# Kernel tuning notes

Hardware: AMD Instinct MI355X
Metric: run time of the kernel (lower is better)

Reference implementation:

```python
import jax, jax.numpy as jnp
import numpy as np

N = 20000      # nodes
E = 640000     # edges (avg degree 32)
H = 128        # hidden_channels
L = 12         # num_layers
DIN = 3        # node feature dim
DE = 4         # edge feature dim
DOUT = 16      # output dim (y_s size)
EPS = 1e-7     # GENConv message eps
LN_EPS = 1e-5


def setup_inputs() -> dict:
    key = jax.random.key(0)
    ks = jax.random.split(key, 12)

    def w(k, shape, fan_in):
        return (jax.random.normal(k, shape, dtype=jnp.float32) / np.float32(np.sqrt(fan_in)))

    return {
        "x": jax.random.normal(ks[0], (N, DIN), dtype=jnp.float32),
        "edge_index": jax.random.randint(ks[1], (2, E), 0, N, dtype=jnp.int32),
        "edge_attr": jax.random.uniform(ks[2], (E, DE), dtype=jnp.float32),
        "enc_node_w": w(ks[3], (DIN, H), DIN),
        "enc_node_b": jnp.zeros((H,), jnp.float32),
        "enc_edge_w": w(ks[4], (DE, H), DE),
        "enc_edge_b": jnp.zeros((H,), jnp.float32),
        "t": jnp.ones((L,), jnp.float32),                 # learnable softmax temperature per layer
        "mlp1_w": w(ks[5], (L, H, 2 * H), H),
        "mlp1_b": jnp.zeros((L, 2 * H), jnp.float32),
        "mlp_ln_g": jnp.ones((L, 2 * H), jnp.float32),
        "mlp_ln_b": jnp.zeros((L, 2 * H), jnp.float32),
        "mlp2_w": w(ks[6], (L, 2 * H, H), 2 * H),
        "mlp2_b": jnp.zeros((L, H), jnp.float32),
        "ln_g": jnp.ones((L, H), jnp.float32),            # DeepGCNLayer pre-norm params
        "ln_b": jnp.zeros((L, H), jnp.float32),
        "lin_w": w(ks[7], (H, DOUT), H),
        "lin_b": jnp.zeros((DOUT,), jnp.float32),
    }


def _layer_norm(x, g, b):
    mu = jnp.mean(x, axis=-1, keepdims=True)
    var = jnp.mean(jnp.square(x - mu), axis=-1, keepdims=True)
    return (x - mu) * jax.lax.rsqrt(var + LN_EPS) * g + b


def _genconv(h, src, dst, ea, ti, w1, b1, g1, bb1, w2, b2):
    # message: relu(x_j + edge_attr) + eps  -> [E, H]
    m = jax.nn.relu(h[src] + ea) + EPS
    # learnable-temperature softmax over edges grouped by destination node
    logits = m * ti
    mx = jax.ops.segment_max(logits, dst, num_segments=N)
    mx = jnp.where(jnp.isfinite(mx), mx, 0.0)  # guard empty segments
    ex = jnp.exp(logits - mx[dst])
    den = jax.ops.segment_sum(ex, dst, num_segments=N) + 1e-16
    agg = jax.ops.segment_sum(m * (ex / den[dst]), dst, num_segments=N)
    # GENConv update: out = MLP(agg + x) with MLP = Lin(H,2H)->LN->ReLU->Lin(2H,H)
    out = agg + h
    u = jax.nn.relu(_layer_norm(out @ w1 + b1, g1, bb1))
    return u @ w2 + b2


def reference(x, edge_index, edge_attr, enc_node_w, enc_node_b, enc_edge_w,
              enc_edge_b, t, mlp1_w, mlp1_b, mlp_ln_g, mlp_ln_b, mlp2_w,
              mlp2_b, ln_g, ln_b, lin_w, lin_b):
    src, dst = edge_index[0], edge_index[1]
    h = x @ enc_node_w + enc_node_b            # node encoder
    ea = edge_attr @ enc_edge_w + enc_edge_b   # edge encoder

    # first layer: conv only (no norm/act, no residual)
    h = _genconv(h, src, dst, ea, t[0], mlp1_w[0], mlp1_b[0], mlp_ln_g[0],
                 mlp_ln_b[0], mlp2_w[0], mlp2_b[0])

    # remaining layers: res+ block  x = x + conv(relu(norm(x)))
    for i in range(1, L):
        hn = jax.nn.relu(_layer_norm(h, ln_g[i], ln_b[i]))
        h = h + _genconv(hn, src, dst, ea, t[i], mlp1_w[i], mlp1_b[i],
                         mlp_ln_g[i], mlp_ln_b[i], mlp2_w[i], mlp2_b[i])

    # final: layers[0].act(layers[0].norm(x)) then output linear
    h = jax.nn.relu(_layer_norm(h, ln_g[0], ln_b[0]))
    return h @ lin_w + lin_b
```

## Files before the change

### kernel.cpp

```cpp
#include <hip/hip_runtime.h>
#include <hip/hip_bf16.h>
#include <math.h>

#define NN 20000
#define EE 640000
#define HH 128
#define LL 12
#define DOUT_ 16
#define EPS_ 1e-7f
#define LN_EPS_ 1e-5f

typedef unsigned short u16;
typedef unsigned int u32;
typedef __attribute__((ext_vector_type(8))) short bf16x8;
typedef __attribute__((ext_vector_type(4))) float f32x4;

__device__ inline u16 bf16_rne(float v) {
  u32 u = __float_as_uint(v);
  return (u16)((u + 0x7FFFu + ((u >> 16) & 1u)) >> 16);
}
__device__ inline float bf16_tof(u16 h) { return __uint_as_float(((u32)h) << 16); }

__global__ __launch_bounds__(256) void hist_kernel(const int* __restrict__ dst, int* __restrict__ deg) {
  int e = blockIdx.x * 256 + threadIdx.x;
  if (e < EE) atomicAdd(&deg[dst[e]], 1);
}

__global__ __launch_bounds__(1024) void scan_kernel(const int* __restrict__ deg, int* __restrict__ off,
                                                    int* __restrict__ cur) {
  __shared__ int part[1024];
  int tid = threadIdx.x;
  const int CH = (NN + 1023) >> 10;
  int base = tid * CH;
  int s = 0;
  for (int j = 0; j < CH; ++j) { int i = base + j; if (i < NN) s += deg[i]; }
  part[tid] = s;
  __syncthreads();
  for (int d = 1; d < 1024; d <<= 1) {
    int v = (tid >= d) ? part[tid - d] : 0;
    __syncthreads();
    part[tid] += v;
    __syncthreads();
  }
  int run = part[tid] - s;
  for (int j = 0; j < CH; ++j) {
    int i = base + j;
    if (i < NN) { off[i] = run; cur[i] = run; run += deg[i]; }
  }
  if (tid == 1023) off[NN] = part[1023];
}

__global__ __launch_bounds__(256) void scatter_kernel(const int* __restrict__ src, const int* __restrict__ dst,
                                                      const float4* __restrict__ ea, int* __restrict__ cur,
                                                      int* __restrict__ srcs, float4* __restrict__ ea4) {
  int e = blockIdx.x * 256 + threadIdx.x;
  if (e >= EE) return;
  int d = dst[e];
  int p = atomicAdd(&cur[d], 1);
  srcs[p] = src[e];
  ea4[p] = ea[e];
}

__global__ __launch_bounds__(256) void wpack_kernel(const float* __restrict__ w, u16* __restrict__ dh,
                                                    u16* __restrict__ dl, int K, int N, int KSC) {
  int fid = blockIdx.x * 256 + threadIdx.x;
  int perL = (K * N) >> 3;
  if (fid >= LL * perL) return;
  int l = fid / perL, r = fid % perL;
  int lane = r & 63;
  int r2 = r >> 6;
  int ks2 = r2 % KSC; r2 /= KSC;
  int NT = N >> 4;
  int tI = r2 % NT;
  int chunk = r2 / NT;
  int c16 = lane & 15, kg = lane >> 4;
  int n = tI * 16 + c16;
  int k0 = (chunk * KSC + ks2) * 32 + kg * 8;
  const float* ws = w + (size_t)l * K * N;
  u16* oh = dh + (size_t)fid * 8;
  u16* ol = dl + (size_t)fid * 8;
  #pragma unroll
  for (int j = 0; j < 8; ++j) {
    float v = ws[(size_t)(k0 + j) * N + n];
    u16 hi = bf16_rne(v);
    oh[j] = hi;
    ol[j] = bf16_rne(v - bf16_tof(hi));
  }
}

__global__ __launch_bounds__(256) void encoder_kernel(const float* __restrict__ x, const float* __restrict__ w,
                                                      const float* __restrict__ b, float* __restrict__ h,
                                                      u16* __restrict__ hb) {
  int id = blockIdx.x * 256 + threadIdx.x;
  if (id >= NN * 64) return;
  int n = id >> 6, cp = id & 63;
  int c0 = cp * 2;
  float x0 = x[n*3+0], x1 = x[n*3+1], x2 = x[n*3+2];
  float vx = b[c0]   + x0*w[c0]   + x1*w[HH+c0]   + x2*w[2*HH+c0];
  float vy = b[c0+1] + x0*w[c0+1] + x1*w[HH+c0+1] + x2*w[2*HH+c0+1];
  *(float2*)&h[(size_t)n*HH + c0] = make_float2(vx, vy);
  *(u32*)&hb[(size_t)n*HH + c0] = (u32)bf16_rne(vx) | ((u32)bf16_rne(vy) << 16);
}

__global__ __launch_bounds__(256) void conv_kernel(const float* __restrict__ hn,
                                                   const u16* __restrict__ hb,
                                                   const int* __restrict__ off,
                                                   const int* __restrict__ srcs, const float4* __restrict__ ea4,
                                                   const float* __restrict__ eew, const float* __restrict__ eeb,
                                                   const float* __restrict__ t, int layer,
                                                   u16* __restrict__ tmpH, u16* __restrict__ tmpL) {
  int wid = blockIdx.x * 4 + (threadIdx.x >> 6);
  int lane = threadIdx.x & 63;
  if (wid >= NN) return;
  int c0 = lane * 2;
  float ti = t[layer];
  float w0x = eew[c0],      w0y = eew[c0+1];
  float w1x = eew[HH+c0],   w1y = eew[HH+c0+1];
  float w2x = eew[2*HH+c0], w2y = eew[2*HH+c0+1];
  float w3x = eew[3*HH+c0], w3y = eew[3*HH+c0+1];
  float bx = eeb[c0], by = eeb[c0+1];
  int e0 = off[wid], e1 = off[wid+1];
  float2 hd = *(const float2*)&hn[(size_t)wid*HH + c0];
  float den0 = 0.f, den1 = 0.f, num0 = 0.f, num1 = 0.f;

  int e = e0;
  const int UF = 8;
  for (; e + UF <= e1; e += UF) {
    int si[UF]; float4 av[UF];
    #pragma unroll
    for (int u = 0; u < UF; ++u) { si[u] = srcs[e + u]; av[u] = ea4[e + u]; }
    u32 hv[UF];
    #pragma unroll
    for (int u = 0; u < UF; ++u) hv[u] = *(const u32*)&hb[((u32)si[u] << 7) + c0];
    #pragma unroll
    for (int u = 0; u < UF; ++u) {
      float hx = bf16_tof((u16)(hv[u] & 0xffffu));
      float hy = bf16_tof((u16)(hv[u] >> 16));
      float eax = fmaf(av[u].w, w3x, fmaf(av[u].z, w2x, fmaf(av[u].y, w1x, fmaf(av[u].x, w0x, bx))));
      float eay = fmaf(av[u].w, w3y, fmaf(av[u].z, w2y, fmaf(av[u].y, w1y, fmaf(av[u].x, w0y, by))));
      float m0 = fmaxf(hx + eax, 0.f) + EPS_;
      float m1 = fmaxf(hy + eay, 0.f) + EPS_;
      float p0 = __expf(m0 * ti);
      float p1 = __expf(m1 * ti);
      den0 += p0; den1 += p1;
      num0 = fmaf(m0, p0, num0);
      num1 = fmaf(m1, p1, num1);
    }
  }
  for (; e < e1; ++e) {
    int sidx = srcs[e];
    float4 a = ea4[e];
    u32 hv = *(const u32*)&hb[((u32)sidx << 7) + c0];
    float hx = bf16_tof((u16)(hv & 0xffffu));
    float hy = bf16_tof((u16)(hv >> 16));
    float eax = fmaf(a.w, w3x, fmaf(a.z, w2x, fmaf(a.y, w1x, fmaf(a.x, w0x, bx))));
    float eay = fmaf(a.w, w3y, fmaf(a.z, w2y, fmaf(a.y, w1y, fmaf(a.x, w0y, by))));
    float m0 = fmaxf(hx + eax, 0.f) + EPS_;
    float m1 = fmaxf(hy + eay, 0.f) + EPS_;
    float p0 = __expf(m0 * ti);
    float p1 = __expf(m1 * ti);
    den0 += p0; den1 += p1;
    num0 = fmaf(m0, p0, num0);
    num1 = fmaf(m1, p1, num1);
  }
  float v0 = num0 / (den0 + 1e-16f) + hd.x;
  float v1 = num1 / (den1 + 1e-16f) + hd.y;
  u16 h0 = bf16_rne(v0), h1 = bf16_rne(v1);
  u16 l0 = bf16_rne(v0 - bf16_tof(h0)), l1 = bf16_rne(v1 - bf16_tof(h1));
  *(u32*)&tmpH[(size_t)wid*HH + c0] = (u32)h0 | ((u32)h1 << 16);
  *(u32*)&tmpL[(size_t)wid*HH + c0] = (u32)l0 | ((u32)l1 << 16);
}

__global__ __launch_bounds__(256) void gemm1_mfma(const u16* __restrict__ Ah, const u16* __restrict__ Al,
                                                  const u16* __restrict__ Bh, const u16* __restrict__ Bl,
                                                  const float* __restrict__ bias,
                                                  const float* __restrict__ g, const float* __restrict__ bb,
                                                  u16* __restrict__ Uh) {
  __shared__ u16 Bs[2][16384];
  int tid = threadIdx.x;
  int wv = tid >> 6, lane = tid & 63;
  int c16 = lane & 15, kg = lane >> 4;
  int row0 = blockIdx.x * 64 + wv * 16;
  int arow = row0 + c16; if (arow > NN - 1) arow = NN - 1;
  const u16* pAh = Ah + (size_t)arow * HH + kg * 8;
  const u16* pAl = Al + (size_t)arow * HH + kg * 8;
  f32x4 acc[16];
  #pragma unroll
  for (int tI = 0; tI < 16; ++tI) acc[tI] = (f32x4){0.f, 0.f, 0.f, 0.f};

  #pragma unroll
  for (int chunk = 0; chunk < 2; ++chunk) {
    const u16* sh = Bh + chunk * 16384;
    const u16* sl = Bl + chunk * 16384;
    #pragma unroll
    for (int it = 0; it < 8; ++it) {
      int idx = (it * 256 + tid) * 8;
      *(f32x4*)&Bs[0][idx] = *(const f32x4*)&sh[idx];
      *(f32x4*)&Bs[1][idx] = *(const f32x4*)&sl[idx];
    }
    __syncthreads();
    #pragma unroll
    for (int ks2 = 0; ks2 < 2; ++ks2) {
      int ks = chunk * 2 + ks2;
      bf16x8 ah = *(const bf16x8*)(pAh + ks * 32);
      bf16x8 al = *(const bf16x8*)(pAl + ks * 32);
      #pragma unroll
      for (int tI = 0; tI < 16; ++tI) {
        int boff = ((tI * 2 + ks2) * 64 + lane) * 8;
        bf16x8 bh = *(const bf16x8*)&Bs[0][boff];
        bf16x8 bl = *(const bf16x8*)&Bs[1][boff];
        acc[tI] = __builtin_amdgcn_mfma_f32_16x16x32_bf16(ah, bh, acc[tI], 0, 0, 0);
        acc[tI] = __builtin_amdgcn_mfma_f32_16x16x32_bf16(al, bh, acc[tI], 0, 0, 0);
        acc[tI] = __builtin_amdgcn_mfma_f32_16x16x32_bf16(ah, bl, acc[tI], 0, 0, 0);
      }
    }
    __syncthreads();
  }

  float bv[16], gv[16], bbv[16];
  #pragma unroll
  for (int tI = 0; tI < 16; ++tI) {
    int c = tI * 16 + c16;
    bv[tI] = bias[c]; gv[tI] = g[c]; bbv[tI] = bb[c];
  }
  #pragma unroll
  for (int j = 0; j < 4; ++j) {
    int row = row0 + kg * 4 + j;
    float xv[16], s = 0.f;
    #pragma unroll
    for (int tI = 0; tI < 16; ++tI) { xv[tI] = acc[tI][j] + bv[tI]; s += xv[tI]; }
    for (int m = 1; m <= 8; m <<= 1) s += __shfl_xor(s, m);
    float mu = s * (1.f / 256.f);
    float q = 0.f;
    #pragma unroll
    for (int tI = 0; tI < 16; ++tI) { xv[tI] -= mu; q += xv[tI] * xv[tI]; }
    for (int m = 1; m <= 8; m <<= 1) q += __shfl_xor(q, m);
    float rs = rsqrtf(q * (1.f / 256.f) + LN_EPS_);
    if (row < NN) {
      #pragma unroll
      for (int tI = 0; tI < 16; ++tI) {
        float o = fmaxf(xv[tI] * rs * gv[tI] + bbv[tI], 0.f);
        Uh[(size_t)row * 256 + tI * 16 + c16] = bf16_rne(o);
      }
    }
  }
}

__global__ __launch_bounds__(256) void gemm2_mfma(const u16* __restrict__ Ah,
                                                  const u16* __restrict__ Bh, const u16* __restrict__ Bl,
                                                  const float* __restrict__ bias,
                                                  const float* __restrict__ gn, const float* __restrict__ bn,
                                                  float* __restrict__ h, float* __restrict__ hnb,
                                                  u16* __restrict__ hb, int first) {
  __shared__ u16 Bs[2][16384];
  int tid = threadIdx.x;
  int wv = tid >> 6, lane = tid & 63;
  int c16 = lane & 15, kg = lane >> 4;
  int row0 = blockIdx.x * 64 + wv * 16;
  int arow = row0 + c16; if (arow > NN - 1) arow = NN - 1;
  const u16* pAh = Ah + (size_t)arow * 256 + kg * 8;
  f32x4 acc[8];
  #pragma unroll
  for (int tI = 0; tI < 8; ++tI) acc[tI] = (f32x4){0.f, 0.f, 0.f, 0.f};

  #pragma unroll
  for (int chunk = 0; chunk < 2; ++chunk) {
    const u16* sh = Bh + chunk * 16384;
    const u16* sl = Bl + chunk * 16384;
    #pragma unroll
    for (int it = 0; it < 8; ++it) {
      int idx = (it * 256 + tid) * 8;
      *(f32x4*)&Bs[0][idx] = *(const f32x4*)&sh[idx];
      *(f32x4*)&Bs[1][idx] = *(const f32x4*)&sl[idx];
    }
    __syncthreads();
    #pragma unroll
    for (int ks2 = 0; ks2 < 4; ++ks2) {
      int ks = chunk * 4 + ks2;
      bf16x8 ah = *(const bf16x8*)(pAh + ks * 32);
      #pragma unroll
      for (int tI = 0; tI < 8; ++tI) {
        int boff = ((tI * 4 + ks2) * 64 + lane) * 8;
        bf16x8 bh = *(const bf16x8*)&Bs[0][boff];
        bf16x8 bl = *(const bf16x8*)&Bs[1][boff];
        acc[tI] = __builtin_amdgcn_mfma_f32_16x16x32_bf16(ah, bh, acc[tI], 0, 0, 0);
        acc[tI] = __builtin_amdgcn_mfma_f32_16x16x32_bf16(ah, bl, acc[tI], 0, 0, 0);
      }
    }
    __syncthreads();
  }

  float bv[8], gv[8], bnv[8];
  #pragma unroll
  for (int tI = 0; tI < 8; ++tI) {
    int c = tI * 16 + c16;
    bv[tI] = bias[c]; gv[tI] = gn[c]; bnv[tI] = bn[c];
  }
  #pragma unroll
  for (int j = 0; j < 4; ++j) {
    int row = row0 + kg * 4 + j;
    bool ok = row < NN;
    float xv[8];
    #pragma unroll
    for (int tI = 0; tI < 8; ++tI) {
      float v = acc[tI][j] + bv[tI];
      if (!first && ok) v += h[(size_t)row * HH + tI * 16 + c16];
      xv[tI] = v;
    }
    if (ok) {
      #pragma unroll
      for (int tI = 0; tI < 8; ++tI) h[(size_t)row * HH + tI * 16 + c16] = xv[tI];
    }
    float s = 0.f;
    #pragma unroll
    for (int tI = 0; tI < 8; ++tI) s += xv[tI];
    for (int m = 1; m <= 8; m <<= 1) s += __shfl_xor(s, m);
    float mu = s * (1.f / 128.f);
    float q = 0.f;
    #pragma unroll
    for (int tI = 0; tI < 8; ++tI) { xv[tI] -= mu; q += xv[tI] * xv[tI]; }
    for (int m = 1; m <= 8; m <<= 1) q += __shfl_xor(q, m);
    float rs = rsqrtf(q * (1.f / 128.f) + LN_EPS_);
    if (ok) {
      #pragma unroll
      for (int tI = 0; tI < 8; ++tI) {
        float o = fmaxf(xv[tI] * rs * gv[tI] + bnv[tI], 0.f);
        size_t p = (size_t)row * HH + tI * 16 + c16;
        hnb[p] = o;
        hb[p] = bf16_rne(o);
      }
    }
  }
}

__global__ __launch_bounds__(256) void outgemm_kernel(const float* __restrict__ hn, const float* __restrict__ w,
                                                      const float* __restrict__ b, float* __restrict__ out) {
  __shared__ float Ws[HH * DOUT_];
  int tid = threadIdx.x;
  {
    const float4* s4 = (const float4*)w;
    float4* d4 = (float4*)Ws;
    d4[tid*2] = s4[tid*2]; d4[tid*2+1] = s4[tid*2+1];
  }
  __syncthreads();
  int id = blockIdx.x * 256 + tid;
  int n = id >> 4, c = id & 15;
  if (n >= NN) return;
  float s = b[c];
  const float* hr = &hn[(size_t)n*HH];
  #pragma unroll 8
  for (int k = 0; k < HH; ++k) s += hr[k] * Ws[k*DOUT_ + c];
  out[n*DOUT_ + c] = s;
}

extern "C" void kernel_launch(void* const* d_in, const int* in_sizes, int n_in,
                              void* d_out, int out_size, void* d_ws, size_t ws_size,
                              hipStream_t stream) {
  const float* x    = (const float*)d_in[0];
  const int*   ei   = (const int*)d_in[1];
  const float* eatt = (const float*)d_in[2];
  const float* enw  = (const float*)d_in[3];
  const float* enb  = (const float*)d_in[4];
  const float* eew  = (const float*)d_in[5];
  const float* eeb  = (const float*)d_in[6];
  const float* t    = (const float*)d_in[7];
  const float* m1w  = (const float*)d_in[8];
  const float* m1b  = (const float*)d_in[9];
  const float* mlg  = (const float*)d_in[10];
  const float* mlb  = (const float*)d_in[11];
  const float* m2w  = (const float*)d_in[12];
  const float* m2b  = (const float*)d_in[13];
  const float* lng  = (const float*)d_in[14];
  const float* lnb  = (const float*)d_in[15];
  const float* linw = (const float*)d_in[16];
  const float* linb = (const float*)d_in[17];
  float* out = (float*)d_out;

  char* ws = (char*)d_ws;
  size_t o = 0;
  auto take = [&](size_t bytes) { char* p = ws + o; o = (o + bytes + 255) & ~(size_t)255; return p; };
  int*    deg  = (int*)take((size_t)NN * 4);
  int*    off  = (int*)take((size_t)(NN + 1) * 4);
  int*    cur  = (int*)take((size_t)NN * 4);
  int*    srcs = (int*)take((size_t)EE * 4);
  float4* ea4  = (float4*)take((size_t)EE * 16);
  float*  h    = (float*)take((size_t)NN * HH * 4);
  float*  hnb  = (float*)take((size_t)NN * HH * 4);
  u16*    hb   = (u16*)take((size_t)NN * HH * 2);
  u16*    tmpH = (u16*)take((size_t)NN * HH * 2);
  u16*    tmpL = (u16*)take((size_t)NN * HH * 2);
  u16*    Uh   = (u16*)take((size_t)NN * 256 * 2);
  u16*    w1h  = (u16*)take((size_t)LL * HH * 256 * 2);
  u16*    w1l  = (u16*)take((size_t)LL * HH * 256 * 2);
  u16*    w2h  = (u16*)take((size_t)LL * 256 * HH * 2);
  u16*    w2l  = (u16*)take((size_t)LL * 256 * HH * 2);

  const int* src = ei;
  const int* dst = ei + EE;

  hipMemsetAsync(deg, 0, (size_t)NN * 4, stream);
  hist_kernel<<<(EE + 255) / 256, 256, 0, stream>>>(dst, deg);
  scan_kernel<<<1, 1024, 0, stream>>>(deg, off, cur);
  scatter_kernel<<<(EE + 255) / 256, 256, 0, stream>>>(src, dst, (const float4*)eatt, cur, srcs, ea4);
  int wblocks = (LL * HH * 256 / 8 + 255) / 256;
  wpack_kernel<<<wblocks, 256, 0, stream>>>(m1w, w1h, w1l, HH, 256, 2);
  wpack_kernel<<<wblocks, 256, 0, stream>>>(m2w, w2h, w2l, 256, HH, 4);
  encoder_kernel<<<(NN * 64 + 255) / 256, 256, 0, stream>>>(x, enw, enb, h, hb);

  int gblocks = (NN + 63) / 64;
  for (int i = 0; i < LL; ++i) {
    const float* cin = (i == 0) ? h : hnb;
    conv_kernel<<<(NN + 3) / 4, 256, 0, stream>>>(cin, hb, off, srcs, ea4, eew, eeb, t, i, tmpH, tmpL);
    gemm1_mfma<<<gblocks, 256, 0, stream>>>(tmpH, tmpL,
                                            w1h + (size_t)i * 32768, w1l + (size_t)i * 32768,
                                            m1b + i * 256, mlg + i * 256, mlb + i * 256, Uh);
    int nrm = (i + 1) % LL;
    gemm2_mfma<<<gblocks, 256, 0, stream>>>(Uh,
                                            w2h + (size_t)i * 32768, w2l + (size_t)i * 32768,
                                            m2b + i * HH, lng + nrm * HH, lnb + nrm * HH,
                                            h, hnb, hb, i == 0 ? 1 : 0);
  }
  outgemm_kernel<<<(NN * DOUT_ + 255) / 256, 256, 0, stream>>>(hnb, linw, linb, out);
}
```

Measured before the change: 1.003 ms.

## Retile MLP GEMMs to 16-row blocks and stage conv edge data in LDS

Both MLP GEMM kernels now use 16-row blocks, with each wave owning a column slice instead of a full row tile. This gives 1250 blocks instead of 313, for better occupancy across CUs. LayerNorm statistics are reduced across waves through shared memory using a sum/sum-of-squares formula, and the weight pack chunking is changed to match. The conv kernel loads each 64-edge batch of source indices and edge attributes cooperatively into LDS and uses exp2 with a prescaled temperature. The trade-off is that each block re-reads the full weight matrix, so B traffic rises, and the one-pass variance is slightly less numerically robust.

```diff
diff --git a/kernel.cpp b/kernel.cpp
--- a/kernel.cpp
+++ b/kernel.cpp
@@ -109,11 +109,14 @@
                                                    const float* __restrict__ eew, const float* __restrict__ eeb,
                                                    const float* __restrict__ t, int layer,
                                                    u16* __restrict__ tmpH, u16* __restrict__ tmpL) {
-  int wid = blockIdx.x * 4 + (threadIdx.x >> 6);
+  __shared__ int    sS[4][64];
+  __shared__ float4 sA[4][64];
+  int w = threadIdx.x >> 6;
+  int wid = blockIdx.x * 4 + w;
   int lane = threadIdx.x & 63;
   if (wid >= NN) return;
   int c0 = lane * 2;
-  float ti = t[layer];
+  float tl = t[layer] * 1.44269504089f;
   float w0x = eew[c0],      w0y = eew[c0+1];
   float w1x = eew[HH+c0],   w1y = eew[HH+c0+1];
   float w2x = eew[2*HH+c0], w2y = eew[2*HH+c0+1];
@@ -123,45 +126,52 @@
   float2 hd = *(const float2*)&hn[(size_t)wid*HH + c0];
   float den0 = 0.f, den1 = 0.f, num0 = 0.f, num1 = 0.f;
 
-  int e = e0;
-  const int UF = 8;
-  for (; e + UF <= e1; e += UF) {
-    int si[UF]; float4 av[UF];
-    #pragma unroll
-    for (int u = 0; u < UF; ++u) { si[u] = srcs[e + u]; av[u] = ea4[e + u]; }
-    u32 hv[UF];
-    #pragma unroll
-    for (int u = 0; u < UF; ++u) hv[u] = *(const u32*)&hb[((u32)si[u] << 7) + c0];
-    #pragma unroll
-    for (int u = 0; u < UF; ++u) {
-      float hx = bf16_tof((u16)(hv[u] & 0xffffu));
-      float hy = bf16_tof((u16)(hv[u] >> 16));
-      float eax = fmaf(av[u].w, w3x, fmaf(av[u].z, w2x, fmaf(av[u].y, w1x, fmaf(av[u].x, w0x, bx))));
-      float eay = fmaf(av[u].w, w3y, fmaf(av[u].z, w2y, fmaf(av[u].y, w1y, fmaf(av[u].x, w0y, by))));
+  for (int base = e0; base < e1; base += 64) {
+    int cnt = e1 - base; if (cnt > 64) cnt = 64;
+    if (lane < cnt) {
+      sS[w][lane] = srcs[base + lane];
+      sA[w][lane] = ea4[base + lane];
+    }
+    int j = 0;
+    const int UF = 8;
+    for (; j + UF <= cnt; j += UF) {
+      int si[UF]; float4 av[UF];
+      #pragma unroll
+      for (int u = 0; u < UF; ++u) { si[u] = sS[w][j+u]; av[u] = sA[w][j+u]; }
+      u32 hv[UF];
+      #pragma unroll
+      for (int u = 0; u < UF; ++u) hv[u] = *(const u32*)&hb[((u32)si[u] << 7) + c0];
+      #pragma unroll
+      for (int u = 0; u < UF; ++u) {
+        float hx = bf16_tof((u16)(hv[u] & 0xffffu));
+        float hy = bf16_tof((u16)(hv[u] >> 16));
+        float eax = fmaf(av[u].w, w3x, fmaf(av[u].z, w2x, fmaf(av[u].y, w1x, fmaf(av[u].x, w0x, bx))));
+        float eay = fmaf(av[u].w, w3y, fmaf(av[u].z, w2y, fmaf(av[u].y, w1y, fmaf(av[u].x, w0y, by))));
+        float m0 = fmaxf(hx + eax, 0.f) + EPS_;
+        float m1 = fmaxf(hy + eay, 0.f) + EPS_;
+        float p0 = exp2f(m0 * tl);
+        float p1 = exp2f(m1 * tl);
+        den0 += p0; den1 += p1;
+        num0 = fmaf(m0, p0, num0);
+        num1 = fmaf(m1, p1, num1);
+      }
+    }
+    for (; j < cnt; ++j) {
+      int sidx = sS[w][j];
+      float4 a = sA[w][j];
+      u32 hv = *(const u32*)&hb[((u32)sidx << 7) + c0];
+      float hx = bf16_tof((u16)(hv & 0xffffu));
+      float hy = bf16_tof((u16)(hv >> 16));
+      float eax = fmaf(a.w, w3x, fmaf(a.z, w2x, fmaf(a.y, w1x, fmaf(a.x, w0x, bx))));
+      float eay = fmaf(a.w, w3y, fmaf(a.z, w2y, fmaf(a.y, w1y, fmaf(a.x, w0y, by))));
       float m0 = fmaxf(hx + eax, 0.f) + EPS_;
       float m1 = fmaxf(hy + eay, 0.f) + EPS_;
-      float p0 = __expf(m0 * ti);
-      float p1 = __expf(m1 * ti);
+      float p0 = exp2f(m0 * tl);
+      float p1 = exp2f(m1 * tl);
       den0 += p0; den1 += p1;
       num0 = fmaf(m0, p0, num0);
       num1 = fmaf(m1, p1, num1);
     }
-  }
-  for (; e < e1; ++e) {
-    int sidx = srcs[e];
-    float4 a = ea4[e];
-    u32 hv = *(const u32*)&hb[((u32)sidx << 7) + c0];
-    float hx = bf16_tof((u16)(hv & 0xffffu));
-    float hy = bf16_tof((u16)(hv >> 16));
-    float eax = fmaf(a.w, w3x, fmaf(a.z, w2x, fmaf(a.y, w1x, fmaf(a.x, w0x, bx))));
-    float eay = fmaf(a.w, w3y, fmaf(a.z, w2y, fmaf(a.y, w1y, fmaf(a.x, w0y, by))));
-    float m0 = fmaxf(hx + eax, 0.f) + EPS_;
-    float m1 = fmaxf(hy + eay, 0.f) + EPS_;
-    float p0 = __expf(m0 * ti);
-    float p1 = __expf(m1 * ti);
-    den0 += p0; den1 += p1;
-    num0 = fmaf(m0, p0, num0);
-    num1 = fmaf(m1, p1, num1);
   }
   float v0 = num0 / (den0 + 1e-16f) + hd.x;
   float v1 = num1 / (den1 + 1e-16f) + hd.y;
@@ -176,72 +186,83 @@
                                                   const float* __restrict__ bias,
                                                   const float* __restrict__ g, const float* __restrict__ bb,
                                                   u16* __restrict__ Uh) {
-  __shared__ u16 Bs[2][16384];
+  __shared__ u16 Bs[2][8192];
+  __shared__ float red[4][16][2];
   int tid = threadIdx.x;
   int wv = tid >> 6, lane = tid & 63;
   int c16 = lane & 15, kg = lane >> 4;
-  int row0 = blockIdx.x * 64 + wv * 16;
-  int arow = row0 + c16; if (arow > NN - 1) arow = NN - 1;
-  const u16* pAh = Ah + (size_t)arow * HH + kg * 8;
-  const u16* pAl = Al + (size_t)arow * HH + kg * 8;
-  f32x4 acc[16];
-  #pragma unroll
-  for (int tI = 0; tI < 16; ++tI) acc[tI] = (f32x4){0.f, 0.f, 0.f, 0.f};
-
-  #pragma unroll
-  for (int chunk = 0; chunk < 2; ++chunk) {
-    const u16* sh = Bh + chunk * 16384;
-    const u16* sl = Bl + chunk * 16384;
-    #pragma unroll
-    for (int it = 0; it < 8; ++it) {
+  int row0 = blockIdx.x * 16;
+  const u16* pAh = Ah + (size_t)(row0 + c16) * HH + kg * 8;
+  const u16* pAl = Al + (size_t)(row0 + c16) * HH + kg * 8;
+  bf16x8 ah[4], al[4];
+  #pragma unroll
+  for (int ks = 0; ks < 4; ++ks) {
+    ah[ks] = *(const bf16x8*)(pAh + ks * 32);
+    al[ks] = *(const bf16x8*)(pAl + ks * 32);
+  }
+  f32x4 acc[4];
+  #pragma unroll
+  for (int i = 0; i < 4; ++i) acc[i] = (f32x4){0.f, 0.f, 0.f, 0.f};
+
+  #pragma unroll
+  for (int ch = 0; ch < 4; ++ch) {
+    const u16* sh = Bh + ch * 8192;
+    const u16* sl = Bl + ch * 8192;
+    #pragma unroll
+    for (int it = 0; it < 4; ++it) {
       int idx = (it * 256 + tid) * 8;
       *(f32x4*)&Bs[0][idx] = *(const f32x4*)&sh[idx];
       *(f32x4*)&Bs[1][idx] = *(const f32x4*)&sl[idx];
     }
     __syncthreads();
     #pragma unroll
-    for (int ks2 = 0; ks2 < 2; ++ks2) {
-      int ks = chunk * 2 + ks2;
-      bf16x8 ah = *(const bf16x8*)(pAh + ks * 32);
-      bf16x8 al = *(const bf16x8*)(pAl + ks * 32);
-      #pragma unroll
-      for (int tI = 0; tI < 16; ++tI) {
-        int boff = ((tI * 2 + ks2) * 64 + lane) * 8;
-        bf16x8 bh = *(const bf16x8*)&Bs[0][boff];
-        bf16x8 bl = *(const bf16x8*)&Bs[1][boff];
-        acc[tI] = __builtin_amdgcn_mfma_f32_16x16x32_bf16(ah, bh, acc[tI], 0, 0, 0);
-        acc[tI] = __builtin_amdgcn_mfma_f32_16x16x32_bf16(al, bh, acc[tI], 0, 0, 0);
-        acc[tI] = __builtin_amdgcn_mfma_f32_16x16x32_bf16(ah, bl, acc[tI], 0, 0, 0);
-      }
-    }
-    __syncthreads();
-  }
-
-  float bv[16], gv[16], bbv[16];
-  #pragma unroll
-  for (int tI = 0; tI < 16; ++tI) {
-    int c = tI * 16 + c16;
-    bv[tI] = bias[c]; gv[tI] = g[c]; bbv[tI] = bb[c];
-  }
+    for (int i = 0; i < 4; ++i) {
+      int boff = ((wv * 4 + i) * 64 + lane) * 8;
+      bf16x8 bh = *(const bf16x8*)&Bs[0][boff];
+      bf16x8 bl = *(const bf16x8*)&Bs[1][boff];
+      acc[i] = __builtin_amdgcn_mfma_f32_16x16x32_bf16(ah[ch], bh, acc[i], 0, 0, 0);
+      acc[i] = __builtin_amdgcn_mfma_f32_16x16x32_bf16(al[ch], bh, acc[i], 0, 0, 0);
+      acc[i] = __builtin_amdgcn_mfma_f32_16x16x32_bf16(ah[ch], bl, acc[i], 0, 0, 0);
+    }
+    __syncthreads();
+  }
+
+  float bv[4], gv[4], bbv[4];
+  #pragma unroll
+  for (int i = 0; i < 4; ++i) {
+    int c = (wv * 4 + i) * 16 + c16;
+    bv[i] = bias[c]; gv[i] = g[c]; bbv[i] = bb[c];
+  }
+  float xv[4][4], s1[4], s2[4];
   #pragma unroll
   for (int j = 0; j < 4; ++j) {
-    int row = row0 + kg * 4 + j;
-    float xv[16], s = 0.f;
-    #pragma unroll
-    for (int tI = 0; tI < 16; ++tI) { xv[tI] = acc[tI][j] + bv[tI]; s += xv[tI]; }
-    for (int m = 1; m <= 8; m <<= 1) s += __shfl_xor(s, m);
-    float mu = s * (1.f / 256.f);
-    float q = 0.f;
-    #pragma unroll
-    for (int tI = 0; tI < 16; ++tI) { xv[tI] -= mu; q += xv[tI] * xv[tI]; }
-    for (int m = 1; m <= 8; m <<= 1) q += __shfl_xor(q, m);
-    float rs = rsqrtf(q * (1.f / 256.f) + LN_EPS_);
-    if (row < NN) {
-      #pragma unroll
-      for (int tI = 0; tI < 16; ++tI) {
-        float o = fmaxf(xv[tI] * rs * gv[tI] + bbv[tI], 0.f);
-        Uh[(size_t)row * 256 + tI * 16 + c16] = bf16_rne(o);
-      }
+    float a1 = 0.f, a2 = 0.f;
+    #pragma unroll
+    for (int i = 0; i < 4; ++i) {
+      float v = acc[i][j] + bv[i];
+      xv[j][i] = v; a1 += v; a2 = fmaf(v, v, a2);
+    }
+    #pragma unroll
+    for (int m = 1; m <= 8; m <<= 1) { a1 += __shfl_xor(a1, m); a2 += __shfl_xor(a2, m); }
+    s1[j] = a1; s2[j] = a2;
+  }
+  if (c16 == 0) {
+    #pragma unroll
+    for (int j = 0; j < 4; ++j) { red[wv][kg*4+j][0] = s1[j]; red[wv][kg*4+j][1] = s2[j]; }
+  }
+  __syncthreads();
+  #pragma unroll
+  for (int j = 0; j < 4; ++j) {
+    int row = kg * 4 + j;
+    float S1 = red[0][row][0] + red[1][row][0] + red[2][row][0] + red[3][row][0];
+    float S2 = red[0][row][1] + red[1][row][1] + red[2][row][1] + red[3][row][1];
+    float mu = S1 * (1.f / 256.f);
+    float var = fmaxf(S2 * (1.f / 256.f) - mu * mu, 0.f);
+    float rs = rsqrtf(var + LN_EPS_);
+    #pragma unroll
+    for (int i = 0; i < 4; ++i) {
+      float o = fmaxf((xv[j][i] - mu) * rs * gv[i] + bbv[i], 0.f);
+      Uh[(size_t)(row0 + row) * 256 + (wv * 4 + i) * 16 + c16] = bf16_rne(o);
     }
   }
 }
@@ -252,83 +273,89 @@
                                                   const float* __restrict__ gn, const float* __restrict__ bn,
                                                   float* __restrict__ h, float* __restrict__ hnb,
                                                   u16* __restrict__ hb, int first) {
-  __shared__ u16 Bs[2][16384];
+  __shared__ u16 Bs[2][8192];
+  __shared__ float red[4][16][2];
   int tid = threadIdx.x;
   int wv = tid >> 6, lane = tid & 63;
   int c16 = lane & 15, kg = lane >> 4;
-  int row0 = blockIdx.x * 64 + wv * 16;
-  int arow = row0 + c16; if (arow > NN - 1) arow = NN - 1;
-  const u16* pAh = Ah + (size_t)arow * 256 + kg * 8;
-  f32x4 acc[8];
-  #pragma unroll
-  for (int tI = 0; tI < 8; ++tI) acc[tI] = (f32x4){0.f, 0.f, 0.f, 0.f};
-
-  #pragma unroll
-  for (int chunk = 0; chunk < 2; ++chunk) {
-    const u16* sh = Bh + chunk * 16384;
-    const u16* sl = Bl + chunk * 16384;
-    #pragma unroll
-    for (int it = 0; it < 8; ++it) {
+  int row0 = blockIdx.x * 16;
+  const u16* pAh = Ah + (size_t)(row0 + c16) * 256 + kg * 8;
+  bf16x8 ah[8];
+  #pragma unroll
+  for (int ks = 0; ks < 8; ++ks) ah[ks] = *(const bf16x8*)(pAh + ks * 32);
+  f32x4 acc[2];
+  #pragma unroll
+  for (int i = 0; i < 2; ++i) acc[i] = (f32x4){0.f, 0.f, 0.f, 0.f};
+
+  #pragma unroll
+  for (int ch = 0; ch < 4; ++ch) {
+    const u16* sh = Bh + ch * 8192;
+    const u16* sl = Bl + ch * 8192;
+    #pragma unroll
+    for (int it = 0; it < 4; ++it) {
       int idx = (it * 256 + tid) * 8;
       *(f32x4*)&Bs[0][idx] = *(const f32x4*)&sh[idx];
       *(f32x4*)&Bs[1][idx] = *(const f32x4*)&sl[idx];
     }
     __syncthreads();
     #pragma unroll
-    for (int ks2 = 0; ks2 < 4; ++ks2) {
-      int ks = chunk * 4 + ks2;
-      bf16x8 ah = *(const bf16x8*)(pAh + ks * 32);
+    for (int ks2 = 0; ks2 < 2; ++ks2) {
+      int ks = ch * 2 + ks2;
       #pragma unroll
-      for (int tI = 0; tI < 8; ++tI) {
-        int boff = ((tI * 4 + ks2) * 64 + lane) * 8;
+      for (int i = 0; i < 2; ++i) {
+        int boff = (((wv * 2 + i) * 2 + ks2) * 64 + lane) * 8;
         bf16x8 bh = *(const bf16x8*)&Bs[0][boff];
         bf16x8 bl = *(const bf16x8*)&Bs[1][boff];
-        acc[tI] = __builtin_amdgcn_mfma_f32_16x16x32_bf16(ah, bh, acc[tI], 0, 0, 0);
-        acc[tI] = __builtin_amdgcn_mfma_f32_16x16x32_bf16(ah, bl, acc[tI], 0, 0, 0);
+        acc[i] = __builtin_amdgcn_mfma_f32_16x16x32_bf16(ah[ks], bh, acc[i], 0, 0, 0);
+        acc[i] = __builtin_amdgcn_mfma_f32_16x16x32_bf16(ah[ks], bl, acc[i], 0, 0, 0);
       }
     }
     __syncthreads();
   }
 
-  float bv[8], gv[8], bnv[8];
-  #pragma unroll
-  for (int tI = 0; tI < 8; ++tI) {
-    int c = tI * 16 + c16;
-    bv[tI] = bias[c]; gv[tI] = gn[c]; bnv[tI] = bn[c];
-  }
+  float bv[2], gv[2], bnv[2];
+  #pragma unroll
+  for (int i = 0; i < 2; ++i) {
+    int c = (wv * 2 + i) * 16 + c16;
+    bv[i] = bias[c]; gv[i] = gn[c]; bnv[i] = bn[c];
+  }
+  float xv[4][2], s1[4], s2[4];
   #pragma unroll
   for (int j = 0; j < 4; ++j) {
     int row = row0 + kg * 4 + j;
-    bool ok = row < NN;
-    float xv[8];
-    #pragma unroll
-    for (int tI = 0; tI < 8; ++tI) {
-      float v = acc[tI][j] + bv[tI];
-      if (!first && ok) v += h[(size_t)row * HH + tI * 16 + c16];
-      xv[tI] = v;
-    }
-    if (ok) {
-      #pragma unroll
-      for (int tI = 0; tI < 8; ++tI) h[(size_t)row * HH + tI * 16 + c16] = xv[tI];
-    }
-    float s = 0.f;
-    #pragma unroll
-    for (int tI = 0; tI < 8; ++tI) s += xv[tI];
-    for (int m = 1; m <= 8; m <<= 1) s += __shfl_xor(s, m);
-    float mu = s * (1.f / 128.f);
-    float q = 0.f;
-    #pragma unroll
-    for (int tI = 0; tI < 8; ++tI) { xv[tI] -= mu; q += xv[tI] * xv[tI]; }
-    for (int m = 1; m <= 8; m <<= 1) q += __shfl_xor(q, m);
-    float rs = rsqrtf(q * (1.f / 128.f) + LN_EPS_);
-    if (ok) {
-      #pragma unroll
-      for (int tI = 0; tI < 8; ++tI) {
-        float o = fmaxf(xv[tI] * rs * gv[tI] + bnv[tI], 0.f);
-        size_t p = (size_t)row * HH + tI * 16 + c16;
-        hnb[p] = o;
-        hb[p] = bf16_rne(o);
-      }
+    float a1 = 0.f, a2 = 0.f;
+    #pragma unroll
+    for (int i = 0; i < 2; ++i) {
+      size_t p = (size_t)row * HH + (wv * 2 + i) * 16 + c16;
+      float v = acc[i][j] + bv[i];
+      if (!first) v += h[p];
+      xv[j][i] = v;
+      h[p] = v;
+      a1 += v; a2 = fmaf(v, v, a2);
+    }
+    #pragma unroll
+    for (int m = 1; m <= 8; m <<= 1) { a1 += __shfl_xor(a1, m); a2 += __shfl_xor(a2, m); }
+    s1[j] = a1; s2[j] = a2;
+  }
+  if (c16 == 0) {
+    #pragma unroll
+    for (int j = 0; j < 4; ++j) { red[wv][kg*4+j][0] = s1[j]; red[wv][kg*4+j][1] = s2[j]; }
+  }
+  __syncthreads();
+  #pragma unroll
+  for (int j = 0; j < 4; ++j) {
+    int row = kg * 4 + j;
+    float S1 = red[0][row][0] + red[1][row][0] + red[2][row][0] + red[3][row][0];
+    float S2 = red[0][row][1] + red[1][row][1] + red[2][row][1] + red[3][row][1];
+    float mu = S1 * (1.f / 128.f);
+    float var = fmaxf(S2 * (1.f / 128.f) - mu * mu, 0.f);
+    float rs = rsqrtf(var + LN_EPS_);
+    #pragma unroll
+    for (int i = 0; i < 2; ++i) {
+      float o = fmaxf((xv[j][i] - mu) * rs * gv[i] + bnv[i], 0.f);
+      size_t p = (size_t)(row0 + row) * HH + (wv * 2 + i) * 16 + c16;
+      hnb[p] = o;
+      hb[p] = bf16_rne(o);
     }
   }
 }
@@ -403,11 +430,11 @@
   scan_kernel<<<1, 1024, 0, stream>>>(deg, off, cur);
   scatter_kernel<<<(EE + 255) / 256, 256, 0, stream>>>(src, dst, (const float4*)eatt, cur, srcs, ea4);
   int wblocks = (LL * HH * 256 / 8 + 255) / 256;
-  wpack_kernel<<<wblocks, 256, 0, stream>>>(m1w, w1h, w1l, HH, 256, 2);
-  wpack_kernel<<<wblocks, 256, 0, stream>>>(m2w, w2h, w2l, 256, HH, 4);
+  wpack_kernel<<<wblocks, 256, 0, stream>>>(m1w, w1h, w1l, HH, 256, 1);
+  wpack_kernel<<<wblocks, 256, 0, stream>>>(m2w, w2h, w2l, 256, HH, 2);
   encoder_kernel<<<(NN * 64 + 255) / 256, 256, 0, stream>>>(x, enw, enb, h, hb);
 
-  int gblocks = (NN + 63) / 64;
+  int gblocks = NN / 16;
   for (int i = 0; i < LL; ++i) {
     const float* cin = (i == 0) ? h : hnb;
     conv_kernel<<<(NN + 3) / 4, 256, 0, stream>>>(cin, hb, off, srcs, ea4, eew, eeb, t, i, tmpH, tmpL);
```

Result: slower. 1.061 ms (+5.8%).
